# Optimization experiments

Measured on AMD Instinct MI355X. Metric: run time of the kernel, lower is better.

Reference implementation:

```python
import jax, jax.numpy as jnp
import numpy as np


def setup_inputs() -> dict:
    key = jax.random.key(0)
    k1, k2, k3 = jax.random.split(key, 3)
    B, Q, K, D = 4, 2048, 2048, 1024
    query = jax.random.normal(k1, (B, Q, D), dtype=jnp.float32)
    value = jax.random.normal(k2, (B, K, D), dtype=jnp.float32)
    attention_mask = jax.random.randint(k3, (B, Q, K), 0, 2, dtype=jnp.int32)
    return {"query": query, "value": value, "attention_mask": attention_mask}


def reference(query, value, attention_mask):
    # key defaults to value in the original module
    D = query.shape[-1]
    # scores[b,q,k] = sum_d (query[b,q,d] + key[b,k,d])
    #              = rowsum(query)[b,q] + rowsum(key)[b,k]  (separable outer-sum,
    # avoids the (B,Q,K,D) intermediate the torch code materializes)
    q_sum = query.sum(-1)                    # (B, Q)
    k_sum = value.sum(-1)                    # (B, K)  (key == value)
    scores = q_sum[:, :, None] + k_sum[:, None, :]   # (B, Q, K)
    scores = scores / jnp.sqrt(jnp.asarray(D, scores.dtype))  # use_scale=True
    mask_value = -1e9
    scores = scores + (1.0 - attention_mask.astype(scores.dtype)) * mask_value
    attention_weights = jax.nn.softmax(scores, axis=-1)       # (B, Q, K)
    context_vector = jnp.einsum('bqk,bkd->bqd', attention_weights, value)
    return (context_vector, attention_weights)
```

## Files before the change

kernel.cpp:

```cpp
#include <hip/hip_runtime.h>
#include <stdint.h>

#define BB 4
#define QQ 2048
#define KK 2048
#define DD 1024

__device__ inline unsigned short f2bf(float f) {
    unsigned int u = __float_as_uint(f);
    unsigned int r = (u + 0x7fffu + ((u >> 16) & 1u)) >> 16;
    return (unsigned short)r;
}

typedef short bf16x8 __attribute__((ext_vector_type(8)));
typedef float f32x4  __attribute__((ext_vector_type(4)));

__device__ inline void async16(const void* g, void* l) {
    __builtin_amdgcn_global_load_lds(
        (const __attribute__((address_space(1))) unsigned int*)g,
        (__attribute__((address_space(3))) unsigned int*)l,
        16, 0, 0);
}

__global__ __launch_bounds__(256) void rowexp(const float* __restrict__ V,
                                              float* __restrict__ e) {
    int wave = threadIdx.x >> 6, lane = threadIdx.x & 63;
    int row = blockIdx.x * 4 + wave;
    const float* p = V + (size_t)row * DD;
    float s = 0.f;
    for (int j = 0; j < 4; j++) {
        float4 v = *(const float4*)(p + j * 256 + lane * 4);
        s += v.x + v.y + v.z + v.w;
    }
    for (int off = 32; off; off >>= 1) s += __shfl_xor(s, off, 64);
    if (lane == 0) e[row] = __expf(s * 0.03125f);
}

__global__ __launch_bounds__(256) void transpose_conv(const float* __restrict__ V,
                                                      unsigned short* __restrict__ Vt) {
    int bid = blockIdx.x;
    int b  = bid >> 9;
    int r  = bid & 511;
    int kt = r >> 4;
    int dt = r & 15;
    int k0 = kt * 64, d0 = dt * 64;
    __shared__ float tile[64 * 65];
    int t = threadIdx.x;
    for (int i = 0; i < 4; i++) {
        int idx = i * 256 + t;
        int row = idx >> 4;
        int c4  = idx & 15;
        float4 v = *(const float4*)(V + (size_t)(b * KK + k0 + row) * DD + d0 + c4 * 4);
        float* p = &tile[row * 65 + c4 * 4];
        p[0] = v.x; p[1] = v.y; p[2] = v.z; p[3] = v.w;
    }
    __syncthreads();
    for (int i = 0; i < 4; i++) {
        int idx = i * 256 + t;
        int dr = idx >> 4;
        int kc = idx & 15;
        ushort4 o;
        o.x = f2bf(tile[(kc * 4 + 0) * 65 + dr]);
        o.y = f2bf(tile[(kc * 4 + 1) * 65 + dr]);
        o.z = f2bf(tile[(kc * 4 + 2) * 65 + dr]);
        o.w = f2bf(tile[(kc * 4 + 3) * 65 + dr]);
        *(ushort4*)(Vt + (size_t)(b * DD + d0 + dr) * KK + k0 + kc * 4) = o;
    }
}

__global__ __launch_bounds__(256) void weights_k(const int* __restrict__ mask,
                                                 const float* __restrict__ e,
                                                 float* __restrict__ wout,
                                                 unsigned short* __restrict__ wb16) {
    int wave = threadIdx.x >> 6, lane = threadIdx.x & 63;
    int row = blockIdx.x * 4 + wave;
    int b = row >> 11;
    const int4*   mp = (const int4*)(mask + (size_t)row * KK);
    const float4* ep = (const float4*)(e + (size_t)b * KK);
    float4 w[8];
    float s = 0.f;
    for (int j = 0; j < 8; j++) {
        int4   m  = mp[lane + j * 64];
        float4 ev = ep[lane + j * 64];
        w[j].x = m.x ? ev.x : 0.f;
        w[j].y = m.y ? ev.y : 0.f;
        w[j].z = m.z ? ev.z : 0.f;
        w[j].w = m.w ? ev.w : 0.f;
        s += (w[j].x + w[j].y) + (w[j].z + w[j].w);
    }
    for (int off = 32; off; off >>= 1) s += __shfl_xor(s, off, 64);
    float rS = 1.f / s;
    float4*  wp = (float4*)(wout + (size_t)row * KK);
    ushort4* bp = (ushort4*)(wb16 + (size_t)row * KK);
    for (int j = 0; j < 8; j++) {
        float4 v = w[j];
        v.x *= rS; v.y *= rS; v.z *= rS; v.w *= rS;
        wp[lane + j * 64] = v;
        ushort4 pk;
        pk.x = f2bf(v.x); pk.y = f2bf(v.y); pk.z = f2bf(v.z); pk.w = f2bf(v.w);
        bp[lane + j * 64] = pk;
    }
}

__global__ __launch_bounds__(256) void gemm_ctx(const unsigned short* __restrict__ Wb,
                                                const unsigned short* __restrict__ Vt,
                                                float* __restrict__ ctx) {
    int bid = blockIdx.x;
    int dt = bid >> 6;
    int b  = (bid >> 4) & 3;
    int qt = bid & 15;
    int q0 = qt * 128, n0 = dt * 128;
    __shared__ unsigned short As[128 * 64];
    __shared__ unsigned short Bs[128 * 64];
    int tid = threadIdx.x, wave = tid >> 6, lane = tid & 63;
    int quad = lane >> 4, lm = lane & 15;
    int wm = wave >> 1, wn = wave & 1;

    int srow   = lane >> 3;
    int schunk = (lane & 7) ^ srow;
    const unsigned short* Ag = Wb + (size_t)(b * QQ + q0 + wave * 8 + srow) * KK + schunk * 8;
    const unsigned short* Bg = Vt + (size_t)(b * DD + n0 + wave * 8 + srow) * KK + schunk * 8;
    unsigned short* lA = &As[(wave * 8) * 64];
    unsigned short* lB = &Bs[(wave * 8) * 64];

    int m7 = lm & 7;
    int xa0 = lm * 64 + ((0 + quad) ^ m7) * 8;
    int xa1 = lm * 64 + ((4 + quad) ^ m7) * 8;

    f32x4 acc[4][4];
    for (int i = 0; i < 4; i++)
        for (int j = 0; j < 4; j++) acc[i][j] = 0.f;

    for (int k0 = 0; k0 < KK; k0 += 64) {
        if (k0) __syncthreads();
        for (int c = 0; c < 4; c++) {
            async16(Ag + (size_t)(c * 32) * KK + k0, lA + c * 32 * 64);
            async16(Bg + (size_t)(c * 32) * KK + k0, lB + c * 32 * 64);
        }
        __syncthreads();
        bf16x8 a[4][2], bv[4][2];
        for (int i = 0; i < 4; i++) {
            a[i][0]  = *(const bf16x8*)&As[(wm * 64 + i * 16) * 64 + xa0];
            a[i][1]  = *(const bf16x8*)&As[(wm * 64 + i * 16) * 64 + xa1];
            bv[i][0] = *(const bf16x8*)&Bs[(wn * 64 + i * 16) * 64 + xa0];
            bv[i][1] = *(const bf16x8*)&Bs[(wn * 64 + i * 16) * 64 + xa1];
        }
        for (int h = 0; h < 2; h++)
            for (int i = 0; i < 4; i++)
                for (int j = 0; j < 4; j++)
                    acc[i][j] = __builtin_amdgcn_mfma_f32_16x16x32_bf16(a[i][h], bv[j][h], acc[i][j], 0, 0, 0);
    }
    for (int i = 0; i < 4; i++) {
        int rowb = q0 + wm * 64 + i * 16 + quad * 4;
        for (int j = 0; j < 4; j++) {
            int col = n0 + wn * 64 + j * 16 + lm;
            for (int rr = 0; rr < 4; rr++)
                ctx[(size_t)(b * QQ + rowb + rr) * DD + col] = acc[i][j][rr];
        }
    }
}

extern "C" void kernel_launch(void* const* d_in, const int* in_sizes, int n_in,
                              void* d_out, int out_size, void* d_ws, size_t ws_size,
                              hipStream_t stream) {
    const float* value = (const float*)d_in[1];
    const int*   mask  = (const int*)d_in[2];
    float* out = (float*)d_out;

    unsigned short* Vt = (unsigned short*)d_ws;
    unsigned short* Wb = Vt + (size_t)BB * DD * KK;
    float* e = (float*)(Wb + (size_t)BB * QQ * KK);

    float* ctx  = out;
    float* wout = out + (size_t)BB * QQ * DD;

    rowexp<<<(BB * KK) / 4, 256, 0, stream>>>(value, e);
    transpose_conv<<<BB * 512, 256, 0, stream>>>(value, Vt);
    weights_k<<<(BB * QQ) / 4, 256, 0, stream>>>(mask, e, wout, Wb);
    gemm_ctx<<<BB * 128, 256, 0, stream>>>(Wb, Vt, ctx);
}
```

Baseline: 243.4 us.

## Fuse row sums into transpose, remap weights blocks, double-buffer GEMM LDS

Row sums of value are now computed as per-tile partials inside the transpose kernel, and a small kernel adds them and exponentiates. This removes the separate full read of value. The weights kernel's block-to-row mapping is permuted, likely to improve cache locality. The context GEMM now double-buffers its LDS tiles so the next k-slice loads while MFMAs run, at the cost of twice the shared memory per block and one barrier per iteration.

```diff
diff --git a/kernel.cpp b/kernel.cpp
--- a/kernel.cpp
+++ b/kernel.cpp
@@ -22,22 +22,9 @@
         16, 0, 0);
 }
 
-__global__ __launch_bounds__(256) void rowexp(const float* __restrict__ V,
-                                              float* __restrict__ e) {
-    int wave = threadIdx.x >> 6, lane = threadIdx.x & 63;
-    int row = blockIdx.x * 4 + wave;
-    const float* p = V + (size_t)row * DD;
-    float s = 0.f;
-    for (int j = 0; j < 4; j++) {
-        float4 v = *(const float4*)(p + j * 256 + lane * 4);
-        s += v.x + v.y + v.z + v.w;
-    }
-    for (int off = 32; off; off >>= 1) s += __shfl_xor(s, off, 64);
-    if (lane == 0) e[row] = __expf(s * 0.03125f);
-}
-
 __global__ __launch_bounds__(256) void transpose_conv(const float* __restrict__ V,
-                                                      unsigned short* __restrict__ Vt) {
+                                                      unsigned short* __restrict__ Vt,
+                                                      float* __restrict__ part) {
     int bid = blockIdx.x;
     int b  = bid >> 9;
     int r  = bid & 511;
@@ -46,13 +33,19 @@
     int k0 = kt * 64, d0 = dt * 64;
     __shared__ float tile[64 * 65];
     int t = threadIdx.x;
+    int g  = t >> 4;
+    int c4 = t & 15;
     for (int i = 0; i < 4; i++) {
-        int idx = i * 256 + t;
-        int row = idx >> 4;
-        int c4  = idx & 15;
+        int row = i * 16 + g;
         float4 v = *(const float4*)(V + (size_t)(b * KK + k0 + row) * DD + d0 + c4 * 4);
         float* p = &tile[row * 65 + c4 * 4];
         p[0] = v.x; p[1] = v.y; p[2] = v.z; p[3] = v.w;
+        float ps = (v.x + v.y) + (v.z + v.w);
+        ps += __shfl_xor(ps, 1, 64);
+        ps += __shfl_xor(ps, 2, 64);
+        ps += __shfl_xor(ps, 4, 64);
+        ps += __shfl_xor(ps, 8, 64);
+        if (c4 == 0) part[(size_t)(b * KK + k0 + row) * 16 + dt] = ps;
     }
     __syncthreads();
     for (int i = 0; i < 4; i++) {
@@ -68,13 +61,29 @@
     }
 }
 
+__global__ __launch_bounds__(256) void expsum(const float* __restrict__ part,
+                                              float* __restrict__ e) {
+    int idx = blockIdx.x * 256 + threadIdx.x;
+    const float4* p = (const float4*)(part + (size_t)idx * 16);
+    float4 a = p[0], bq = p[1], c = p[2], d = p[3];
+    float s = ((a.x + a.y) + (a.z + a.w)) + ((bq.x + bq.y) + (bq.z + bq.w))
+            + ((c.x + c.y) + (c.z + c.w)) + ((d.x + d.y) + (d.z + d.w));
+    e[idx] = __expf(s * 0.03125f);
+}
+
 __global__ __launch_bounds__(256) void weights_k(const int* __restrict__ mask,
                                                  const float* __restrict__ e,
                                                  float* __restrict__ wout,
                                                  unsigned short* __restrict__ wb16) {
+    int bid = blockIdx.x;
+    int qlow  = bid & 7;
+    int rest  = bid >> 3;
+    int sub   = rest & 31;
+    int qhigh = (rest >> 5) & 1;
+    int b     = rest >> 6;
+    int qt    = qhigh * 8 + qlow;
     int wave = threadIdx.x >> 6, lane = threadIdx.x & 63;
-    int row = blockIdx.x * 4 + wave;
-    int b = row >> 11;
+    int row = b * QQ + qt * 128 + sub * 4 + wave;
     const int4*   mp = (const int4*)(mask + (size_t)row * KK);
     const float4* ep = (const float4*)(e + (size_t)b * KK);
     float4 w[8];
@@ -110,8 +119,8 @@
     int b  = (bid >> 4) & 3;
     int qt = bid & 15;
     int q0 = qt * 128, n0 = dt * 128;
-    __shared__ unsigned short As[128 * 64];
-    __shared__ unsigned short Bs[128 * 64];
+    __shared__ unsigned short As[2][128 * 64];
+    __shared__ unsigned short Bs[2][128 * 64];
     int tid = threadIdx.x, wave = tid >> 6, lane = tid & 63;
     int quad = lane >> 4, lm = lane & 15;
     int wm = wave >> 1, wn = wave & 1;
@@ -120,8 +129,7 @@
     int schunk = (lane & 7) ^ srow;
     const unsigned short* Ag = Wb + (size_t)(b * QQ + q0 + wave * 8 + srow) * KK + schunk * 8;
     const unsigned short* Bg = Vt + (size_t)(b * DD + n0 + wave * 8 + srow) * KK + schunk * 8;
-    unsigned short* lA = &As[(wave * 8) * 64];
-    unsigned short* lB = &Bs[(wave * 8) * 64];
+    int lbase = (wave * 8) * 64;
 
     int m7 = lm & 7;
     int xa0 = lm * 64 + ((0 + quad) ^ m7) * 8;
@@ -131,19 +139,29 @@
     for (int i = 0; i < 4; i++)
         for (int j = 0; j < 4; j++) acc[i][j] = 0.f;
 
-    for (int k0 = 0; k0 < KK; k0 += 64) {
-        if (k0) __syncthreads();
-        for (int c = 0; c < 4; c++) {
-            async16(Ag + (size_t)(c * 32) * KK + k0, lA + c * 32 * 64);
-            async16(Bg + (size_t)(c * 32) * KK + k0, lB + c * 32 * 64);
+    for (int c = 0; c < 4; c++) {
+        async16(Ag + (size_t)(c * 32) * KK, &As[0][lbase + c * 32 * 64]);
+        async16(Bg + (size_t)(c * 32) * KK, &Bs[0][lbase + c * 32 * 64]);
+    }
+
+    for (int it = 0; it < 32; it++) {
+        __syncthreads();
+        if (it + 1 < 32) {
+            int k0 = (it + 1) * 64;
+            int nb = (it + 1) & 1;
+            for (int c = 0; c < 4; c++) {
+                async16(Ag + (size_t)(c * 32) * KK + k0, &As[nb][lbase + c * 32 * 64]);
+                async16(Bg + (size_t)(c * 32) * KK + k0, &Bs[nb][lbase + c * 32 * 64]);
+            }
         }
-        __syncthreads();
+        const unsigned short* A = As[it & 1];
+        const unsigned short* B = Bs[it & 1];
         bf16x8 a[4][2], bv[4][2];
         for (int i = 0; i < 4; i++) {
-            a[i][0]  = *(const bf16x8*)&As[(wm * 64 + i * 16) * 64 + xa0];
-            a[i][1]  = *(const bf16x8*)&As[(wm * 64 + i * 16) * 64 + xa1];
-            bv[i][0] = *(const bf16x8*)&Bs[(wn * 64 + i * 16) * 64 + xa0];
-            bv[i][1] = *(const bf16x8*)&Bs[(wn * 64 + i * 16) * 64 + xa1];
+            a[i][0]  = *(const bf16x8*)&A[(wm * 64 + i * 16) * 64 + xa0];
+            a[i][1]  = *(const bf16x8*)&A[(wm * 64 + i * 16) * 64 + xa1];
+            bv[i][0] = *(const bf16x8*)&B[(wn * 64 + i * 16) * 64 + xa0];
+            bv[i][1] = *(const bf16x8*)&B[(wn * 64 + i * 16) * 64 + xa1];
         }
         for (int h = 0; h < 2; h++)
             for (int i = 0; i < 4; i++)
@@ -169,13 +187,14 @@
 
     unsigned short* Vt = (unsigned short*)d_ws;
     unsigned short* Wb = Vt + (size_t)BB * DD * KK;
-    float* e = (float*)(Wb + (size_t)BB * QQ * KK);
+    float* e    = (float*)(Wb + (size_t)BB * QQ * KK);
+    float* part = e + BB * KK;
 
     float* ctx  = out;
     float* wout = out + (size_t)BB * QQ * DD;
 
-    rowexp<<<(BB * KK) / 4, 256, 0, stream>>>(value, e);
-    transpose_conv<<<BB * 512, 256, 0, stream>>>(value, Vt);
+    transpose_conv<<<BB * 512, 256, 0, stream>>>(value, Vt, part);
+    expsum<<<(BB * KK) / 256, 256, 0, stream>>>(part, e);
     weights_k<<<(BB * QQ) / 4, 256, 0, stream>>>(mask, e, wout, Wb);
     gemm_ctx<<<BB * 128, 256, 0, stream>>>(Wb, Vt, ctx);
 }
```

New measurement: 253.2 us. 1.04x slower.
